# Kernel optimization log

Hardware: AMD Instinct MI355X
Metric: run time of the kernel (lower is better)

The kernel has to match this reference:

```python
import jax, jax.numpy as jnp
import numpy as np
import math

L = 6      # num transformer layers
D = 128    # hidden_dim
H = 8      # heads
C = D // H # per-head dim (concat -> H*C == hidden_dim so residual add works)
F = 9      # node_features
OUT = 3    # output_dim
B, S, NN = 2, 128, 64
N = B * S * NN
E = 262144


def setup_inputs() -> dict:
    key = jax.random.key(0)
    ks = jax.random.split(key, 16)
    sc = 0.02
    g = lambda k, shp: jax.random.normal(k, shp, jnp.float32) * sc

    x = jax.random.normal(ks[0], (N, F), jnp.float32)
    edge_index = jax.random.randint(ks[1], (2, E), 0, N, dtype=jnp.int32)

    # sinusoidal positional encoding buffer [S, D]
    pos = np.arange(S, dtype=np.float32)[:, None]
    div = np.exp(np.arange(0, D, 2, dtype=np.float32) * (-math.log(10000.0) / D))
    pe = np.zeros((S, D), np.float32)
    pe[:, 0::2] = np.sin(pos * div)
    pe[:, 1::2] = np.cos(pos * div)

    return dict(
        x=x, edge_index=edge_index, pe=jnp.asarray(pe),
        Win=g(ks[2], (F, D)), bin_=jnp.zeros((D,), jnp.float32),
        Wq=g(ks[3], (L, D, D)), bq=jnp.zeros((L, D), jnp.float32),
        Wk=g(ks[4], (L, D, D)), bk=jnp.zeros((L, D), jnp.float32),
        Wv=g(ks[5], (L, D, D)), bv=jnp.zeros((L, D), jnp.float32),
        Ws=g(ks[6], (L, D, D)), bs=jnp.zeros((L, D), jnp.float32),
        Wb=g(ks[7], (L, 3 * D, 1)), bb=jnp.zeros((L, 1), jnp.float32),
        ln_g=jnp.ones((L, D), jnp.float32), ln_b=jnp.zeros((L, D), jnp.float32),
        Wo1=g(ks[8], (D, D // 2)), bo1=jnp.zeros((D // 2,), jnp.float32),
        Wo2=g(ks[9], (D // 2, OUT)), bo2=jnp.zeros((OUT,), jnp.float32),
        batch_size=B, seq_len=S, num_nodes=NN,
    )


def _layer_norm(x, g, b, eps=1e-5):
    mu = x.mean(-1, keepdims=True)
    var = ((x - mu) ** 2).mean(-1, keepdims=True)
    return (x - mu) / jnp.sqrt(var + eps) * g + b


def _transformer_conv(h, src, dst, Wq, bq, Wk, bk, Wv, bv, Ws, bs, Wb, bb):
    # PyG TransformerConv (beta=True, concat): edge gather -> per-head dot scores
    # -> scatter-softmax over incoming edges per dst node -> scatter-add aggregate.
    n = h.shape[0]
    q = (h @ Wq + bq).reshape(n, H, C)
    k = (h @ Wk + bk).reshape(n, H, C)
    v = (h @ Wv + bv).reshape(n, H, C)
    scores = jnp.einsum('ehc,ehc->eh', q[dst], k[src]) / math.sqrt(C)  # [E,H]
    m = jax.ops.segment_max(scores, dst, num_segments=n)               # [N,H]
    ex = jnp.exp(scores - jax.lax.stop_gradient(m)[dst])
    denom = jax.ops.segment_sum(ex, dst, num_segments=n)
    alpha = ex / (denom[dst] + 1e-16)                                  # [E,H]
    msg = (v[src] * alpha[:, :, None]).reshape(-1, H * C)              # [E,D]
    agg = jax.ops.segment_sum(msg, dst, num_segments=n)                # [N,D]
    xr = h @ Ws + bs                                                   # skip branch
    beta = jax.nn.sigmoid(jnp.concatenate([agg, xr, agg - xr], -1) @ Wb + bb)
    return beta * xr + (1.0 - beta) * agg


def reference(x, edge_index, pe, Win, bin_, Wq, bq, Wk, bk, Wv, bv, Ws, bs,
              Wb, bb, ln_g, ln_b, Wo1, bo1, Wo2, bo2,
              batch_size, seq_len, num_nodes):
    src, dst = edge_index[0], edge_index[1]
    d = Win.shape[1]
    h = x @ Win + bin_
    # add temporal positional encoding per timestep
    h = (h.reshape(batch_size, seq_len, num_nodes, d)
         + pe[:seq_len][None, :, None, :]).reshape(-1, d)
    for i in range(Wq.shape[0]):
        hn = _transformer_conv(h, src, dst, Wq[i], bq[i], Wk[i], bk[i],
                               Wv[i], bv[i], Ws[i], bs[i], Wb[i], bb[i])
        h = _layer_norm(h + hn, ln_g[i], ln_b[i])
    return jax.nn.relu(h @ Wo1 + bo1) @ Wo2 + bo2
```

## Files before the change

### kernel.cpp

```cpp
#include <hip/hip_runtime.h>

#define NNODES 16384
#define EDGES  262144
#define DH     128
#define NH     8
#define CH     16
#define NL     6
#define SEQ    128
#define NNPG   64

#define PBLK   768
#define PTHR   (PBLK * 256)
#define PWAV   (PBLK * 4)

typedef short bf16x8 __attribute__((ext_vector_type(8)));
typedef float f32x4 __attribute__((ext_vector_type(4)));
typedef float f32x2 __attribute__((ext_vector_type(2)));

static __device__ __forceinline__ unsigned short f2bf(float f) {
  unsigned u = __float_as_uint(f);
  u += 0x7FFFu + ((u >> 16) & 1u);
  return (unsigned short)(u >> 16);
}
static __device__ __forceinline__ float bfl(unsigned u) { return __uint_as_float(u << 16); }
static __device__ __forceinline__ float bfh(unsigned u) { return __uint_as_float(u & 0xffff0000u); }
static __device__ __forceinline__ f32x2 mk2(float x, float y) { f32x2 t; t[0] = x; t[1] = y; return t; }

__global__ __launch_bounds__(256) void k_pro(const int* __restrict__ ei,
    int* __restrict__ cnt, int* __restrict__ csr_pad,
    const float* __restrict__ Wq, const float* __restrict__ Wk,
    const float* __restrict__ Wv, const float* __restrict__ Ws,
    unsigned short* __restrict__ Wf,
    const float* __restrict__ x, const float* __restrict__ Win,
    const float* __restrict__ bin, const float* __restrict__ pe,
    float* __restrict__ h, unsigned short* __restrict__ hb) {
  const int tid = threadIdx.x;
  const int lane = tid & 63, wid = tid >> 6;
  const int gtid = blockIdx.x * 256 + tid;
  const int gw = blockIdx.x * 4 + wid;

  for (int e = gtid; e < EDGES; e += PTHR) {
    const int d = ei[EDGES + e];
    const int s = ei[e];
    const int slot = atomicAdd(&cnt[d], 1);
    if (slot < 64) csr_pad[d * 64 + (slot & 7) * 8 + (slot >> 3)] = s;
  }

  if (gw < NL * 128) {
    const int layer = gw >> 7, rem = gw & 127;
    const int mat = rem >> 5, tile = rem & 31;
    const int nt = tile >> 2, kt = tile & 3;
    const float* W = ((mat == 0) ? Wq : (mat == 1) ? Wk : (mat == 2) ? Wv : Ws)
                     + layer * DH * DH;
    const int nn = nt * 16 + (lane & 15);
    const int k0 = kt * 32 + (lane >> 4) * 8;
    unsigned pk[4];
#pragma unroll
    for (int jj = 0; jj < 4; ++jj) {
      const unsigned lo = f2bf(W[(k0 + 2 * jj) * DH + nn]);
      const unsigned hi = f2bf(W[(k0 + 2 * jj + 1) * DH + nn]);
      pk[jj] = lo | (hi << 16);
    }
    uint4 o = {pk[0], pk[1], pk[2], pk[3]};
    *(uint4*)&Wf[(((layer * 4 + mat) * 32 + tile) * 64 + lane) * 8] = o;
  }

  for (int n = gw; n < NNODES; n += PWAV) {
    const int d0 = lane * 2;
    float xs[9];
#pragma unroll
    for (int f = 0; f < 9; ++f) xs[f] = x[n * 9 + f];
    float a0 = bin[d0], a1 = bin[d0 + 1];
#pragma unroll
    for (int f = 0; f < 9; ++f) {
      const float2 w = *(const float2*)&Win[f * DH + d0];
      a0 = fmaf(xs[f], w.x, a0);
      a1 = fmaf(xs[f], w.y, a1);
    }
    const float2 pev = *(const float2*)&pe[((n / NNPG) % SEQ) * DH + d0];
    const float v0 = a0 + pev.x, v1 = a1 + pev.y;
    float2 hv = {v0, v1};
    *(float2*)&h[n * DH + d0] = hv;
    *(unsigned*)&hb[n * DH + d0] = (unsigned)f2bf(v0) | ((unsigned)f2bf(v1) << 16);
  }
}

__global__ __launch_bounds__(512, 2) void k_gemm(const unsigned short* __restrict__ hb,
    const unsigned short* __restrict__ Wf,
    const float* __restrict__ bq, const float* __restrict__ bk,
    const float* __restrict__ bv, const float* __restrict__ bs,
    unsigned short* __restrict__ qb, unsigned char* __restrict__ kv8,
    float* __restrict__ xr) {
  __shared__ uint4 As4[512];
  const int mt = blockIdx.x;
  const int wv = threadIdx.x >> 6, lane = threadIdx.x & 63;
  {
    const int t = threadIdx.x;
    const int row = t >> 4, cb = t & 15;
    As4[t] = *(const uint4*)&hb[(mt * 32 + row) * DH + ((cb ^ (row & 7)) * 8)];
  }
  __syncthreads();

  const int cg = wv;
  const int mat = cg >> 1, nbase = (cg & 1) * 64;
  const unsigned short* Wm = Wf + mat * 16384;
  const float* bias = (mat == 0) ? bq : (mat == 1) ? bk : (mat == 2) ? bv : bs;
  const int m0 = lane & 15, quad = lane >> 4;
  const int nt0 = (cg & 1) * 4;
  const char* Asb = (const char*)As4;

  const f32x4 z = {0.f, 0.f, 0.f, 0.f};
  f32x4 acc[2][4] = {{z, z, z, z}, {z, z, z, z}};
#pragma unroll
  for (int kt = 0; kt < 4; ++kt) {
    const int cbr = kt * 4 + quad;
    const bf16x8 a0 = *(const bf16x8*)(Asb + m0 * 256 + ((cbr ^ (m0 & 7)) * 16));
    const bf16x8 a1 = *(const bf16x8*)(Asb + (16 + m0) * 256 + ((cbr ^ (m0 & 7)) * 16));
#pragma unroll
    for (int j = 0; j < 4; ++j) {
      const bf16x8 b = *(const bf16x8*)&Wm[(((nt0 + j) * 4 + kt) * 64 + lane) * 8];
      acc[0][j] = __builtin_amdgcn_mfma_f32_16x16x32_bf16(a0, b, acc[0][j], 0, 0, 0);
      acc[1][j] = __builtin_amdgcn_mfma_f32_16x16x32_bf16(a1, b, acc[1][j], 0, 0, 0);
    }
  }
  const int kvoff = (mat == 1) ? 0 : 16;
#pragma unroll
  for (int half = 0; half < 2; ++half) {
#pragma unroll
    for (int j = 0; j < 4; ++j) {
      const int col = nbase + j * 16 + m0;
      const float bvv = bias[col];
#pragma unroll
      for (int r = 0; r < 4; ++r) {
        const float val = acc[half][j][r] + bvv;
        const int row = mt * 32 + half * 16 + quad * 4 + r;
        if (mat == 0) {
          qb[row * DH + col] = f2bf(val);
        } else if (mat == 3) {
          xr[row * DH + col] = val;
        } else {
          const float nbv = __shfl_xor(val, 1);
          if ((lane & 1) == 0) {
            const int pk = __builtin_amdgcn_cvt_pk_fp8_f32(val, nbv, 0, false);
            const int head = col >> 4, dim = col & 15;
            *(unsigned short*)&kv8[row * 256 + head * 32 + kvoff + dim] =
                (unsigned short)pk;
          }
        }
      }
    }
  }
}

__device__ __forceinline__ void decode16bf2(const uint4 a, const uint4 b, f32x2* r) {
  r[0] = mk2(bfl(a.x), bfh(a.x)); r[1] = mk2(bfl(a.y), bfh(a.y));
  r[2] = mk2(bfl(a.z), bfh(a.z)); r[3] = mk2(bfl(a.w), bfh(a.w));
  r[4] = mk2(bfl(b.x), bfh(b.x)); r[5] = mk2(bfl(b.y), bfh(b.y));
  r[6] = mk2(bfl(b.z), bfh(b.z)); r[7] = mk2(bfl(b.w), bfh(b.w));
}

__device__ __forceinline__ void decode8x2(const uint4 u, f32x2* r) {
  r[0] = __builtin_amdgcn_cvt_pk_f32_fp8(u.x, false);
  r[1] = __builtin_amdgcn_cvt_pk_f32_fp8(u.x, true);
  r[2] = __builtin_amdgcn_cvt_pk_f32_fp8(u.y, false);
  r[3] = __builtin_amdgcn_cvt_pk_f32_fp8(u.y, true);
  r[4] = __builtin_amdgcn_cvt_pk_f32_fp8(u.z, false);
  r[5] = __builtin_amdgcn_cvt_pk_f32_fp8(u.z, true);
  r[6] = __builtin_amdgcn_cvt_pk_f32_fp8(u.w, false);
  r[7] = __builtin_amdgcn_cvt_pk_f32_fp8(u.w, true);
}

__device__ __forceinline__ void edge_acc2(const uint4 ku, const uint4 vu, bool valid,
    const f32x2* __restrict__ q2, f32x2* __restrict__ a2, float& denom) {
  f32x2 kr[8];
  decode8x2(ku, kr);
  f32x2 d2 = mk2(0.f, 0.f);
#pragma unroll
  for (int c = 0; c < 8; ++c) d2 = d2 + q2[c] * kr[c];
  const float dot = d2[0] + d2[1];
  const float ex = valid ? __expf(dot * 0.25f) : 0.f;
  denom += ex;
  f32x2 vr[8];
  decode8x2(vu, vr);
  const f32x2 e2 = mk2(ex, ex);
#pragma unroll
  for (int c = 0; c < 8; ++c) a2[c] = a2[c] + e2 * vr[c];
}

template <bool LAST>
__global__ __launch_bounds__(512, 2) void k_layer(
    const unsigned short* __restrict__ qb_i, const unsigned char* __restrict__ kv8_i,
    const int* __restrict__ degv, const int* __restrict__ csr_pad,
    float* __restrict__ h, const float* __restrict__ xr_i,
    const float* __restrict__ Wb, const float* __restrict__ bb,
    const float* __restrict__ ln_g, const float* __restrict__ ln_b,
    const unsigned short* __restrict__ Wfn, const float* __restrict__ bqn,
    const float* __restrict__ bkn, const float* __restrict__ bvn,
    const float* __restrict__ bsn,
    unsigned short* __restrict__ qb_o, unsigned char* __restrict__ kv8_o,
    float* __restrict__ xr_o,
    const float* __restrict__ Wo1, const float* __restrict__ bo1,
    const float* __restrict__ Wo2, const float* __restrict__ bo2,
    float* __restrict__ out) {
  __shared__ float hsf[32][DH];
  const int wv = threadIdx.x >> 6, lane = threadIdx.x & 63;
  const int nb = blockIdx.x * 32;
  const int es = lane >> 3, hd = lane & 7;
  const int d0 = hd * CH + es * 2;
  const float2 lw0 = *(const float2*)&Wb[d0];
  const float2 lw1 = *(const float2*)&Wb[DH + d0];
  const float2 lw2 = *(const float2*)&Wb[2 * DH + d0];
  const float2 lg = *(const float2*)&ln_g[d0];
  const float2 lb = *(const float2*)&ln_b[d0];
  const float bbv = bb[0];

  const int n0 = nb + wv * 4;
  int4 iv = *(const int4*)&csr_pad[n0 * 64 + es * 8];
  int deg = degv[n0];
  const uint4* qp0 = (const uint4*)&qb_i[n0 * DH + hd * CH];
  uint4 qa = qp0[0], qc = qp0[1];
  float2 xrv = *(const float2*)&xr_i[n0 * DH + d0];
  float2 hv = *(const float2*)&h[n0 * DH + d0];

#pragma unroll
  for (int t4 = 0; t4 < 4; ++t4) {
    const int row = wv * 4 + t4;
    const int n = nb + row;
    int ntb = (deg + 7) >> 3;
    if (ntb > 8) ntb = 8;
    const int idx[4] = {iv.x, iv.y, iv.z, iv.w};
    bool valv[4];
#pragma unroll
    for (int t = 0; t < 4; ++t) valv[t] = (es + 8 * t) < deg;
    uint4 kf[4], vf[4];
#pragma unroll
    for (int t = 0; t < 4; ++t) {
      if (t < ntb) {
        const int s = valv[t] ? idx[t] : 0;
        const unsigned char* base = &kv8_i[s * 256 + hd * 32];
        kf[t] = *(const uint4*)base;
        vf[t] = *(const uint4*)(base + 16);
      }
    }
    int4 iv_n = iv;
    int deg_n = deg;
    uint4 qa_n = qa, qc_n = qc;
    float2 xrv_n = xrv, hv_n = hv;
    if (t4 < 3) {
      const int nn = n + 1;
      iv_n = *(const int4*)&csr_pad[nn * 64 + es * 8];
      deg_n = degv[nn];
      const uint4* qp = (const uint4*)&qb_i[nn * DH + hd * CH];
      qa_n = qp[0];
      qc_n = qp[1];
      xrv_n = *(const float2*)&xr_i[nn * DH + d0];
      hv_n = *(const float2*)&h[nn * DH + d0];
    }
    f32x2 q2[8];
    decode16bf2(qa, qc, q2);
    f32x2 a2[8];
#pragma unroll
    for (int c = 0; c < 8; ++c) a2[c] = mk2(0.f, 0.f);
    float denom = 0.f;
#pragma unroll
    for (int t = 0; t < 4; ++t) {
      if (t < ntb) edge_acc2(kf[t], vf[t], valv[t], q2, a2, denom);
    }
    for (int t = 4; t < ntb; ++t) {
      const bool v = (es + 8 * t) < deg;
      const int s = v ? csr_pad[n * 64 + es * 8 + t] : 0;
      const unsigned char* base = &kv8_i[s * 256 + hd * 32];
      const uint4 ku = *(const uint4*)base;
      const uint4 vu = *(const uint4*)(base + 16);
      edge_acc2(ku, vu, v, q2, a2, denom);
    }
#pragma unroll
    for (int off = 8; off <= 32; off <<= 1) denom += __shfl_xor(denom, off);
    const bool hi32 = (lane & 32) != 0;
    f32x2 r4[4];
#pragma unroll
    for (int c = 0; c < 4; ++c) {
      const f32x2 keep = hi32 ? a2[c + 4] : a2[c];
      const f32x2 send = hi32 ? a2[c] : a2[c + 4];
      const f32x2 rec = mk2(__shfl_xor(send[0], 32), __shfl_xor(send[1], 32));
      r4[c] = keep + rec;
    }
    const bool hi16 = (lane & 16) != 0;
    f32x2 r2[2];
#pragma unroll
    for (int c = 0; c < 2; ++c) {
      const f32x2 keep = hi16 ? r4[c + 2] : r4[c];
      const f32x2 send = hi16 ? r4[c] : r4[c + 2];
      const f32x2 rec = mk2(__shfl_xor(send[0], 16), __shfl_xor(send[1], 16));
      r2[c] = keep + rec;
    }
    const bool hi8 = (lane & 8) != 0;
    f32x2 rr;
    {
      const f32x2 keep = hi8 ? r2[1] : r2[0];
      const f32x2 send = hi8 ? r2[0] : r2[1];
      const f32x2 rec = mk2(__shfl_xor(send[0], 8), __shfl_xor(send[1], 8));
      rr = keep + rec;
    }
    const float inv = 1.f / (denom + 1e-16f);
    const float ax = rr[0] * inv, ay = rr[1] * inv;
    float p = ax * lw0.x + ay * lw0.y + xrv.x * lw1.x + xrv.y * lw1.y
            + (ax - xrv.x) * lw2.x + (ay - xrv.y) * lw2.y;
#pragma unroll
    for (int off = 1; off <= 32; off <<= 1) p += __shfl_xor(p, off);
    const float beta = 1.f / (1.f + __expf(-(p + bbv)));
    const float t0 = hv.x + beta * xrv.x + (1.f - beta) * ax;
    const float t1 = hv.y + beta * xrv.y + (1.f - beta) * ay;
    float sum = t0 + t1, sq = t0 * t0 + t1 * t1;
#pragma unroll
    for (int off = 1; off <= 32; off <<= 1) {
      sum += __shfl_xor(sum, off);
      sq  += __shfl_xor(sq, off);
    }
    const float mu = sum * (1.f / DH);
    const float rinv = rsqrtf(sq * (1.f / DH) - mu * mu + 1e-5f);
    const float2 o = {(t0 - mu) * rinv * lg.x + lb.x, (t1 - mu) * rinv * lg.y + lb.y};
    if constexpr (!LAST) {
      *(float2*)&h[n * DH + d0] = o;
      const int cb = 2 * hd + (es >> 2);
      *(unsigned*)((char*)hsf + row * 256 + ((cb ^ (row & 7)) * 16) + (es & 3) * 4) =
          (unsigned)f2bf(o.x) | ((unsigned)f2bf(o.y) << 16);
    } else {
      hsf[row][d0] = o.x;
      hsf[row][d0 + 1] = o.y;
    }
    iv = iv_n; deg = deg_n; qa = qa_n; qc = qc_n; xrv = xrv_n; hv = hv_n;
  }
  __syncthreads();

  if constexpr (!LAST) {
    const int cg = wv;
    const int mat = cg >> 1, nbase = (cg & 1) * 64;
    const unsigned short* Wm = Wfn + mat * 16384;
    const float* bias = (mat == 0) ? bqn : (mat == 1) ? bkn : (mat == 2) ? bvn : bsn;
    const int m0 = lane & 15, quad = lane >> 4;
    const int nt0 = (cg & 1) * 4;
    const char* Asb = (const char*)hsf;
    const f32x4 z = {0.f, 0.f, 0.f, 0.f};
    f32x4 acc[2][4] = {{z, z, z, z}, {z, z, z, z}};
#pragma unroll
    for (int kt = 0; kt < 4; ++kt) {
      const int cbr = kt * 4 + quad;
      const bf16x8 a0 = *(const bf16x8*)(Asb + m0 * 256 + ((cbr ^ (m0 & 7)) * 16));
      const bf16x8 a1 = *(const bf16x8*)(Asb + (16 + m0) * 256 + ((cbr ^ (m0 & 7)) * 16));
#pragma unroll
      for (int j = 0; j < 4; ++j) {
        const bf16x8 b = *(const bf16x8*)&Wm[(((nt0 + j) * 4 + kt) * 64 + lane) * 8];
        acc[0][j] = __builtin_amdgcn_mfma_f32_16x16x32_bf16(a0, b, acc[0][j], 0, 0, 0);
        acc[1][j] = __builtin_amdgcn_mfma_f32_16x16x32_bf16(a1, b, acc[1][j], 0, 0, 0);
      }
    }
    const int kvoff = (mat == 1) ? 0 : 16;
#pragma unroll
    for (int half = 0; half < 2; ++half) {
#pragma unroll
      for (int j = 0; j < 4; ++j) {
        const int col = nbase + j * 16 + m0;
        const float bvv = bias[col];
#pragma unroll
        for (int r = 0; r < 4; ++r) {
          const float val = acc[half][j][r] + bvv;
          const int row = nb + half * 16 + quad * 4 + r;
          if (mat == 0) {
            qb_o[row * DH + col] = f2bf(val);
          } else if (mat == 3) {
            xr_o[row * DH + col] = val;
          } else {
            const float nbv = __shfl_xor(val, 1);
            if ((lane & 1) == 0) {
              const int pk = __builtin_amdgcn_cvt_pk_fp8_f32(val, nbv, 0, false);
              const int head = col >> 4, dim = col & 15;
              *(unsigned short*)&kv8_o[row * 256 + head * 32 + kvoff + dim] =
                  (unsigned short)pk;
            }
          }
        }
      }
    }
  } else {
    for (int t4 = 0; t4 < 4; ++t4) {
      const int row = wv * 4 + t4;
      const int n = nb + row;
      float m = bo1[lane];
#pragma unroll 16
      for (int d = 0; d < DH; ++d) m = fmaf(hsf[row][d], Wo1[d * 64 + lane], m);
      m = fmaxf(m, 0.f);
      float o0 = m * Wo2[lane * 3 + 0];
      float o1 = m * Wo2[lane * 3 + 1];
      float o2 = m * Wo2[lane * 3 + 2];
#pragma unroll
      for (int off = 32; off; off >>= 1) {
        o0 += __shfl_xor(o0, off);
        o1 += __shfl_xor(o1, off);
        o2 += __shfl_xor(o2, off);
      }
      if (lane == 0) {
        out[n * 3 + 0] = o0 + bo2[0];
        out[n * 3 + 1] = o1 + bo2[1];
        out[n * 3 + 2] = o2 + bo2[2];
      }
    }
  }
}

extern "C" void kernel_launch(void* const* d_in, const int* in_sizes, int n_in,
                              void* d_out, int out_size, void* d_ws, size_t ws_size,
                              hipStream_t stream) {
  const float* x   = (const float*)d_in[0];
  const int*   ei  = (const int*)d_in[1];
  const float* pe  = (const float*)d_in[2];
  const float* Win = (const float*)d_in[3];
  const float* bin = (const float*)d_in[4];
  const float* Wq  = (const float*)d_in[5];
  const float* bq  = (const float*)d_in[6];
  const float* Wk  = (const float*)d_in[7];
  const float* bk  = (const float*)d_in[8];
  const float* Wv  = (const float*)d_in[9];
  const float* bv  = (const float*)d_in[10];
  const float* Wsk = (const float*)d_in[11];
  const float* bs  = (const float*)d_in[12];
  const float* Wb  = (const float*)d_in[13];
  const float* bb  = (const float*)d_in[14];
  const float* lng = (const float*)d_in[15];
  const float* lnb = (const float*)d_in[16];
  const float* Wo1 = (const float*)d_in[17];
  const float* bo1 = (const float*)d_in[18];
  const float* Wo2 = (const float*)d_in[19];
  const float* bo2 = (const float*)d_in[20];

  const size_t NU = (size_t)NNODES * DH;
  char* base = (char*)d_ws;
  float* h   = (float*)base;                  base += NU * 4;
  unsigned short* hb = (unsigned short*)base; base += NU * 2;
  unsigned short* Wf = (unsigned short*)base; base += (size_t)NL * 4 * 16384 * 2;
  int* cnt     = (int*)base;                  base += NNODES * 4;
  int* csr_pad = (int*)base;                  base += (size_t)NNODES * 64 * 4;
  float* xrA = (float*)base;                  base += NU * 4;
  float* xrB = (float*)base;                  base += NU * 4;
  unsigned short* qbA = (unsigned short*)base; base += NU * 2;
  unsigned short* qbB = (unsigned short*)base; base += NU * 2;
  unsigned char* kvA = (unsigned char*)base;  base += NU * 2;
  unsigned char* kvB = (unsigned char*)base;  base += NU * 2;

  (void)hipMemsetAsync(cnt, 0, NNODES * sizeof(int), stream);
  k_pro<<<PBLK, 256, 0, stream>>>(ei, cnt, csr_pad, Wq, Wk, Wv, Wsk, Wf,
                                  x, Win, bin, pe, h, hb);
  k_gemm<<<NNODES / 32, 512, 0, stream>>>(hb, Wf, bq, bk, bv, bs, qbA, kvA, xrA);
  for (int l = 0; l < NL - 1; ++l) {
    const bool even = (l & 1) == 0;
    k_layer<false><<<NNODES / 32, 512, 0, stream>>>(
        even ? qbA : qbB, even ? kvA : kvB, cnt, csr_pad, h, even ? xrA : xrB,
        Wb + l * 3 * DH, bb + l, lng + l * DH, lnb + l * DH,
        Wf + (size_t)(l + 1) * 4 * 16384,
        bq + (l + 1) * DH, bk + (l + 1) * DH, bv + (l + 1) * DH, bs + (l + 1) * DH,
        even ? qbB : qbA, even ? kvB : kvA, even ? xrB : xrA,
        Wo1, bo1, Wo2, bo2, (float*)d_out);
  }
  k_layer<true><<<NNODES / 32, 512, 0, stream>>>(
      qbB, kvB, cnt, csr_pad, h, xrB,
      Wb + 5 * 3 * DH, bb + 5, lng + 5 * DH, lnb + 5 * DH,
      Wf, bq, bk, bv, bs, qbA, kvA, xrA,
      Wo1, bo1, Wo2, bo2, (float*)d_out);
}
```

Measured before the change: 316.6 us.

## Software-pipeline K/V edge gathers one node ahead with double-buffered registers

Restructures the per-wave 4-node loop so the K/V gathers for the next node are issued before the current node's attention math, using ping-pong register buffers (kfA/kfB). CSR indices and degrees are now prefetched two nodes ahead. The aim is to hide gather latency behind compute. The cost is higher register pressure from holding two sets of 8 uint4 fragments, which could reduce occupancy.

```diff
diff --git a/kernel.cpp b/kernel.cpp
--- a/kernel.cpp
+++ b/kernel.cpp
@@ -213,49 +213,72 @@
   const float2 lg = *(const float2*)&ln_g[d0];
   const float2 lb = *(const float2*)&ln_b[d0];
   const float bbv = bb[0];
-
   const int n0 = nb + wv * 4;
-  int4 iv = *(const int4*)&csr_pad[n0 * 64 + es * 8];
-  int deg = degv[n0];
+
+  int4 iv0 = *(const int4*)&csr_pad[n0 * 64 + es * 8];
+  int4 iv1 = *(const int4*)&csr_pad[(n0 + 1) * 64 + es * 8];
+  int deg0 = degv[n0], deg1 = degv[n0 + 1];
   const uint4* qp0 = (const uint4*)&qb_i[n0 * DH + hd * CH];
   uint4 qa = qp0[0], qc = qp0[1];
   float2 xrv = *(const float2*)&xr_i[n0 * DH + d0];
   float2 hv = *(const float2*)&h[n0 * DH + d0];
 
-#pragma unroll
-  for (int t4 = 0; t4 < 4; ++t4) {
+  uint4 kfA[4], vfA[4], kfB[4], vfB[4];
+  {
+    int ntbg = (deg0 + 7) >> 3;
+    if (ntbg > 4) ntbg = 4;
+    const int idx[4] = {iv0.x, iv0.y, iv0.z, iv0.w};
+#pragma unroll
+    for (int t = 0; t < 4; ++t) {
+      if (t < ntbg) {
+        const bool v = (es + 8 * t) < deg0;
+        const int s = v ? idx[t] : 0;
+        const unsigned char* base = &kv8_i[s * 256 + hd * 32];
+        kfA[t] = *(const uint4*)base;
+        vfA[t] = *(const uint4*)(base + 16);
+      }
+    }
+  }
+
+  auto iter = [&](uint4 (&kfc)[4], uint4 (&vfc)[4],
+                  uint4 (&kfn)[4], uint4 (&vfn)[4], int t4) {
     const int row = wv * 4 + t4;
     const int n = nb + row;
-    int ntb = (deg + 7) >> 3;
-    if (ntb > 8) ntb = 8;
-    const int idx[4] = {iv.x, iv.y, iv.z, iv.w};
-    bool valv[4];
-#pragma unroll
-    for (int t = 0; t < 4; ++t) valv[t] = (es + 8 * t) < deg;
-    uint4 kf[4], vf[4];
-#pragma unroll
-    for (int t = 0; t < 4; ++t) {
-      if (t < ntb) {
-        const int s = valv[t] ? idx[t] : 0;
-        const unsigned char* base = &kv8_i[s * 256 + hd * 32];
-        kf[t] = *(const uint4*)base;
-        vf[t] = *(const uint4*)(base + 16);
-      }
-    }
-    int4 iv_n = iv;
-    int deg_n = deg;
+    if (t4 < 3) {
+      int ntbg = (deg1 + 7) >> 3;
+      if (ntbg > 4) ntbg = 4;
+      const int idxn[4] = {iv1.x, iv1.y, iv1.z, iv1.w};
+#pragma unroll
+      for (int t = 0; t < 4; ++t) {
+        if (t < ntbg) {
+          const bool v = (es + 8 * t) < deg1;
+          const int s = v ? idxn[t] : 0;
+          const unsigned char* base = &kv8_i[s * 256 + hd * 32];
+          kfn[t] = *(const uint4*)base;
+          vfn[t] = *(const uint4*)(base + 16);
+        }
+      }
+    }
+    int4 iv2 = iv1;
+    int deg2 = deg1;
+    if (t4 < 2) {
+      iv2 = *(const int4*)&csr_pad[(n + 2) * 64 + es * 8];
+      deg2 = degv[n + 2];
+    }
     uint4 qa_n = qa, qc_n = qc;
-    float2 xrv_n = xrv, hv_n = hv;
+    float2 xr_n = xrv, hv_n = hv;
     if (t4 < 3) {
-      const int nn = n + 1;
-      iv_n = *(const int4*)&csr_pad[nn * 64 + es * 8];
-      deg_n = degv[nn];
-      const uint4* qp = (const uint4*)&qb_i[nn * DH + hd * CH];
+      const uint4* qp = (const uint4*)&qb_i[(n + 1) * DH + hd * CH];
       qa_n = qp[0];
       qc_n = qp[1];
-      xrv_n = *(const float2*)&xr_i[nn * DH + d0];
-      hv_n = *(const float2*)&h[nn * DH + d0];
-    }
+      xr_n = *(const float2*)&xr_i[(n + 1) * DH + d0];
+      hv_n = *(const float2*)&h[(n + 1) * DH + d0];
+    }
+    int ntb = (deg0 + 7) >> 3;
+    if (ntb > 8) ntb = 8;
+    bool valv[4];
+#pragma unroll
+    for (int t = 0; t < 4; ++t) valv[t] = (es + 8 * t) < deg0;
     f32x2 q2[8];
     decode16bf2(qa, qc, q2);
     f32x2 a2[8];
@@ -264,10 +287,10 @@
     float denom = 0.f;
 #pragma unroll
     for (int t = 0; t < 4; ++t) {
-      if (t < ntb) edge_acc2(kf[t], vf[t], valv[t], q2, a2, denom);
+      if (t < ntb) edge_acc2(kfc[t], vfc[t], valv[t], q2, a2, denom);
     }
     for (int t = 4; t < ntb; ++t) {
-      const bool v = (es + 8 * t) < deg;
+      const bool v = (es + 8 * t) < deg0;
       const int s = v ? csr_pad[n * 64 + es * 8 + t] : 0;
       const unsigned char* base = &kv8_i[s * 256 + hd * 32];
       const uint4 ku = *(const uint4*)base;
@@ -329,8 +352,14 @@
       hsf[row][d0] = o.x;
       hsf[row][d0 + 1] = o.y;
     }
-    iv = iv_n; deg = deg_n; qa = qa_n; qc = qc_n; xrv = xrv_n; hv = hv_n;
-  }
+    iv0 = iv1; deg0 = deg1;
+    iv1 = iv2; deg1 = deg2;
+    qa = qa_n; qc = qc_n; xrv = xr_n; hv = hv_n;
+  };
+  iter(kfA, vfA, kfB, vfB, 0);
+  iter(kfB, vfB, kfA, vfA, 1);
+  iter(kfA, vfA, kfB, vfB, 2);
+  iter(kfB, vfB, kfA, vfA, 3);
   __syncthreads();
 
   if constexpr (!LAST) {
```

Measured after the change: 331.6 us. 4.7% more time.
